# Performance work log

Measured on AMD Instinct MI355X. Metric: run time of the kernel, lower is better.

## Reference

```python
import jax, jax.numpy as jnp
import numpy as np
from jax import lax

EPS = 1e-12

def _ln(x, bias):
    # zero_mean=False, scale=False LayerNorm: RMS-style normalize + bias
    var = jnp.mean(x * x, axis=-1, keepdims=True)
    return x / jnp.sqrt(var + EPS) + bias

def _lru(h, nu_log, theta_log, b_re, b_im, c_re, c_im, d):
    # h: [B,S,H]; diagonal complex linear recurrence (LRU)
    lam = jnp.exp(-jnp.exp(nu_log) + 1j * jnp.exp(theta_log))  # [U] complex
    gamma = jnp.sqrt(jnp.clip(1.0 - jnp.abs(lam) ** 2, 0.0, None)).astype(h.dtype)  # [U]
    Bu = (jnp.einsum('bsh,uh->bsu', h, b_re) + 1j * jnp.einsum('bsh,uh->bsu', h, b_im)) * gamma  # [B,S,U]
    a = jnp.broadcast_to(lam, Bu.shape)
    def binop(e1, e2):
        a1, x1 = e1
        a2, x2 = e2
        return a1 * a2, a2 * x1 + x2
    _, states = lax.associative_scan(binop, (a, Bu), axis=1)  # [B,S,U] complex
    y = (jnp.einsum('bsu,hu->bsh', jnp.real(states), c_re)
         - jnp.einsum('bsu,hu->bsh', jnp.imag(states), c_im))
    return y + d * h

def setup_inputs() -> dict:
    key = jax.random.key(0)
    ks = jax.random.split(key, 12)
    B, S, H, L, F, V, P = 4, 2048, 1024, 4, 4096, 32000, 2048
    s = 0.02
    return {
        'input_ids': jax.random.randint(ks[0], (B, S), 0, V),
        'word_emb': jax.random.normal(ks[1], (V, H), jnp.float32) * s,
        'pos_emb': jax.random.normal(ks[2], (P, H), jnp.float32) * s,
        'nu_log': jax.random.normal(ks[3], (L, H), jnp.float32) * 0.5,
        'theta_log': jax.random.normal(ks[4], (L, H), jnp.float32) * 0.5,
        'B_re': jax.random.normal(ks[5], (L, H, H), jnp.float32) / np.sqrt(H),
        'B_im': jax.random.normal(ks[6], (L, H, H), jnp.float32) / np.sqrt(H),
        'C_re': jax.random.normal(ks[7], (L, H, H), jnp.float32) / np.sqrt(H),
        'C_im': jax.random.normal(ks[8], (L, H, H), jnp.float32) / np.sqrt(H),
        'D': jax.random.normal(ks[9], (L, H), jnp.float32),
        'rnn_norm_bias': jnp.zeros((L, H), jnp.float32),
        'w1': jax.random.normal(ks[10], (L, F, H), jnp.float32) * s,
        'b1': jnp.zeros((L, F), jnp.float32),
        'w2': jax.random.normal(ks[11], (L, H, F), jnp.float32) * s,
        'b2': jnp.zeros((L, H), jnp.float32),
        'ffn_norm_bias': jnp.zeros((L, H), jnp.float32),
    }

def reference(input_ids, word_emb, pos_emb, nu_log, theta_log, B_re, B_im,
              C_re, C_im, D, rnn_norm_bias, w1, b1, w2, b2, ffn_norm_bias):
    S = input_ids.shape[1]
    pos_ids = jnp.arange(S)
    h = word_emb[input_ids] + pos_emb[pos_ids][None, :, :]  # [B,S,H]
    L = nu_log.shape[0]
    for l in range(L):
        rnn_out = _lru(h, nu_log[l], theta_log[l], B_re[l], B_im[l], C_re[l], C_im[l], D[l])
        h = _ln(h + rnn_out, rnn_norm_bias[l])
        ffn = jnp.einsum('bsf,hf->bsh',
                         jax.nn.gelu(jnp.einsum('bsh,fh->bsf', h, w1[l]) + b1[l], approximate=False),
                         w2[l]) + b2[l]
        h = _ln(h + ffn, ffn_norm_bias[l])
    return h
```

## Files before the change

### kernel.cpp

```cpp
#include <hip/hip_runtime.h>
#include <hip/hip_bf16.h>
#include <math.h>

typedef __attribute__((ext_vector_type(8))) short short8;
typedef __attribute__((ext_vector_type(4))) float f32x4;

__device__ __forceinline__ float bf2f(unsigned short u) {
  union { unsigned int i; float f; } v; v.i = ((unsigned int)u) << 16; return v.f;
}
__device__ __forceinline__ unsigned short f2bf(float f) {
  union { float f; unsigned int i; } v; v.f = f;
  unsigned int r = v.i + 0x7fffu + ((v.i >> 16) & 1u);
  return (unsigned short)(r >> 16);
}
__device__ __forceinline__ uint4 cvt8(const float* __restrict__ src, float scale) {
  float4 a = *(const float4*)src;
  float4 b = *(const float4*)(src + 4);
  uint4 o; unsigned short* op = (unsigned short*)&o;
  op[0] = f2bf(a.x * scale); op[1] = f2bf(a.y * scale);
  op[2] = f2bf(a.z * scale); op[3] = f2bf(a.w * scale);
  op[4] = f2bf(b.x * scale); op[5] = f2bf(b.y * scale);
  op[6] = f2bf(b.z * scale); op[7] = f2bf(b.w * scale);
  return o;
}
__device__ __forceinline__ void glds16(const unsigned short* g, unsigned short* s) {
  __builtin_amdgcn_global_load_lds(
      (const __attribute__((address_space(1))) unsigned int*)g,
      (__attribute__((address_space(3))) unsigned int*)s, 16, 0, 0);
}

__global__ void embed_k(const int* __restrict__ ids, const float* __restrict__ we,
                        const float* __restrict__ pe, unsigned short* __restrict__ h) {
  int t = blockIdx.x * 256 + threadIdx.x;
  int c8 = (t & 127) * 8, row = t >> 7;
  int s = row & 2047;
  int id = ids[row];
  const float* ap = we + (size_t)id * 1024 + c8;
  const float* bp = pe + (size_t)s * 1024 + c8;
  float4 a0 = *(const float4*)ap, a1 = *(const float4*)(ap + 4);
  float4 b0 = *(const float4*)bp, b1 = *(const float4*)(bp + 4);
  uint4 o; unsigned short* op = (unsigned short*)&o;
  op[0] = f2bf(a0.x + b0.x); op[1] = f2bf(a0.y + b0.y);
  op[2] = f2bf(a0.z + b0.z); op[3] = f2bf(a0.w + b0.w);
  op[4] = f2bf(a1.x + b1.x); op[5] = f2bf(a1.y + b1.y);
  op[6] = f2bf(a1.z + b1.z); op[7] = f2bf(a1.w + b1.w);
  *(uint4*)(h + (size_t)row * 1024 + c8) = o;
}

__global__ void prep_lam_k(const float* __restrict__ nu_log,
                           const float* __restrict__ theta_log,
                           float* __restrict__ lamP) {
  int t = blockIdx.x * 256 + threadIdx.x;
  float nu = nu_log[t], th = theta_log[t];
  float mag = expf(-expf(nu));
  float eth = expf(th);
  float lr = mag * cosf(eth), li = mag * sinf(eth);
  float g2 = 1.0f - mag * mag; if (g2 < 0.f) g2 = 0.f;
  float pr = 1.f, pi = 0.f;
#pragma unroll 1
  for (int i = 0; i < 64; ++i) { float nr = pr * lr - pi * li; pi = pr * li + pi * lr; pr = nr; }
  lamP[t] = lr;
  lamP[4096 + t] = li;
  lamP[2 * 4096 + t] = sqrtf(g2);
  lamP[3 * 4096 + t] = pr;
  lamP[4 * 4096 + t] = pi;
}

__global__ void prep_w_k(const float* __restrict__ Bre, const float* __restrict__ Bim,
                         const float* __restrict__ Cre, const float* __restrict__ Cim,
                         const float* __restrict__ gamma, unsigned short* __restrict__ Bw,
                         unsigned short* __restrict__ Cw) {
  int t = blockIdx.x * 256 + threadIdx.x;
  if (t < 262144) {
    int n = t >> 7, h8 = (t & 127) * 8;
    int u = n & 1023;
    const float* src = (n < 1024 ? Bre : Bim) + (size_t)u * 1024 + h8;
    *(uint4*)(Bw + (size_t)n * 1024 + h8) = cvt8(src, gamma[u]);
  } else {
    int t2 = t - 262144;
    int hrow = t2 >> 8, u8 = (t2 & 255) * 8;
    uint4 o;
    if (u8 < 1024) o = cvt8(Cre + (size_t)hrow * 1024 + u8, 1.0f);
    else           o = cvt8(Cim + (size_t)hrow * 1024 + (u8 - 1024), -1.0f);
    *(uint4*)(Cw + (size_t)hrow * 2048 + u8) = o;
  }
}

__global__ void prep_ffn_k(const float* __restrict__ w1l, const float* __restrict__ w2l,
                           unsigned short* __restrict__ w1b, unsigned short* __restrict__ w2b) {
  int t = blockIdx.x * 256 + threadIdx.x;
  size_t off = (size_t)t * 8;
  if (t < 524288) {
    *(uint4*)(w1b + off) = cvt8(w1l + off, 1.0f);
  } else {
    size_t o2 = off - 4194304;
    *(uint4*)(w2b + o2) = cvt8(w2l + o2, 1.0f);
  }
}

template <int EPI>
__global__ __launch_bounds__(256, 2) void gemm_nt(
    const unsigned short* __restrict__ A, const unsigned short* __restrict__ Bm,
    void* __restrict__ Cout, const float* __restrict__ bias, int M, int N, int K) {
  __shared__ unsigned short As[2 * 128 * 32];
  __shared__ unsigned short Bs[2 * 128 * 32];
  const int tid = threadIdx.x;
  const int lane = tid & 63;
  const int wave = tid >> 6;
  const int quad = lane >> 4, r = lane & 15;
  const int wm = (wave >> 1) * 64, wn = (wave & 1) * 64;
  const size_t row0 = (size_t)blockIdx.x * 128;
  const size_t col0 = (size_t)blockIdx.y * 128;
  const unsigned short* Ab = A + row0 * K;
  const unsigned short* Bb = Bm + col0 * K;
  const int li0 = tid, li1 = 256 + tid;
  const int rw0 = li0 >> 2, sg0 = (li0 & 3) * 8;
  const int rw1 = li1 >> 2, sg1 = (li1 & 3) * 8;
  unsigned short* As0 = As + wave * 512;
  unsigned short* Bs0 = Bs + wave * 512;
  unsigned short* As1 = As + 2048 + wave * 512;
  unsigned short* Bs1 = Bs + 2048 + wave * 512;
  const unsigned short* Ap0 = Ab + (size_t)rw0 * K + sg0;
  const unsigned short* Bp0 = Bb + (size_t)rw0 * K + sg0;
  const unsigned short* Ap1 = Ab + (size_t)rw1 * K + sg1;
  const unsigned short* Bp1 = Bb + (size_t)rw1 * K + sg1;

  f32x4 acc[4][4];
#pragma unroll
  for (int i = 0; i < 4; ++i)
#pragma unroll
    for (int j = 0; j < 4; ++j) acc[i][j] = (f32x4){0.f, 0.f, 0.f, 0.f};

  glds16(Ap0, As0);
  glds16(Bp0, Bs0);
  glds16(Ap1, As1);
  glds16(Bp1, Bs1);
  __syncthreads();

  const int nk = K >> 5;
  int cur = 0;
  for (int t = 0; t < nk; ++t) {
    if (t + 1 < nk) {
      const int kn = (t + 1) << 5;
      const int nb = (cur ^ 1) * 4096;
      glds16(Ap0 + kn, As0 + nb);
      glds16(Bp0 + kn, Bs0 + nb);
      glds16(Ap1 + kn, As1 + nb);
      glds16(Bp1 + kn, Bs1 + nb);
    }
    const unsigned short* Ac = As + cur * 4096;
    const unsigned short* Bc = Bs + cur * 4096;
    short8 aF[4], bF[4];
#pragma unroll
    for (int i = 0; i < 4; ++i) aF[i] = *(const short8*)(Ac + (wm + i * 16 + r) * 32 + quad * 8);
#pragma unroll
    for (int j = 0; j < 4; ++j) bF[j] = *(const short8*)(Bc + (wn + j * 16 + r) * 32 + quad * 8);
#pragma unroll
    for (int i = 0; i < 4; ++i)
#pragma unroll
      for (int j = 0; j < 4; ++j)
        acc[i][j] = __builtin_amdgcn_mfma_f32_16x16x32_bf16(aF[i], bF[j], acc[i][j], 0, 0, 0);
    __syncthreads();
    cur ^= 1;
  }
  unsigned short* Cb = (unsigned short*)Cout;
  float* Cf = (float*)Cout;
#pragma unroll
  for (int j = 0; j < 4; ++j) {
    const size_t gcol = col0 + wn + j * 16 + r;
    float bv = 0.f;
    if (EPI == 2 || EPI == 3) bv = bias[gcol];
#pragma unroll
    for (int i = 0; i < 4; ++i) {
      const size_t grow = row0 + wm + i * 16 + quad * 4;
#pragma unroll
      for (int tt = 0; tt < 4; ++tt) {
        float v = acc[i][j][tt] + bv;
        size_t idx = (grow + tt) * (size_t)N + gcol;
        if (EPI == 2) {
          v = 0.5f * v * (1.0f + erff(v * 0.70710678118654752f));
          Cb[idx] = f2bf(v);
        } else if (EPI == 0) {
          Cb[idx] = f2bf(v);
        } else {
          Cf[idx] = v;
        }
      }
    }
  }
}

__global__ void scan_carry_k(const unsigned short* __restrict__ Bu, const float* __restrict__ lamP,
                             float* __restrict__ carry, int l) {
  int t = blockIdx.x * 256 + threadIdx.x;
  int u = t & 1023, c = (t >> 10) & 31, b = t >> 15;
  float lr = lamP[l * 1024 + u], li = lamP[4096 + l * 1024 + u];
  const unsigned short* base = Bu + ((size_t)(b * 2048 + c * 64)) * 2048 + u;
  float sr = 0.f, si = 0.f;
  for (int g = 0; g < 4; ++g) {
#pragma unroll
    for (int j = 0; j < 16; ++j) {
      size_t off = (size_t)(g * 16 + j) * 2048;
      float vr = bf2f(base[off]), vi = bf2f(base[off + 1024]);
      float nr = lr * sr - li * si + vr;
      si = lr * si + li * sr + vi;
      sr = nr;
    }
  }
  size_t idx = ((size_t)b * 32 + c) * 1024 + u;
  carry[idx] = sr; carry[131072 + idx] = si;
}

__global__ void scan_comb_k(const float* __restrict__ carry, const float* __restrict__ lamP,
                            float* __restrict__ inst, int l) {
  int t = blockIdx.x * 256 + threadIdx.x;
  int u = t & 1023, b = t >> 10;
  float tr = lamP[3 * 4096 + l * 1024 + u], ti = lamP[4 * 4096 + l * 1024 + u];
  float pr = 0.f, pi = 0.f;
  for (int c = 0; c < 32; ++c) {
    size_t idx = ((size_t)b * 32 + c) * 1024 + u;
    inst[idx] = pr; inst[131072 + idx] = pi;
    float cr = carry[idx], ci = carry[131072 + idx];
    float nr = tr * pr - ti * pi + cr;
    pi = tr * pi + ti * pr + ci;
    pr = nr;
  }
}

__global__ void scan_final_k(unsigned short* __restrict__ Bu, const float* __restrict__ lamP,
                             const float* __restrict__ inst, int l) {
  int t = blockIdx.x * 256 + threadIdx.x;
  int u = t & 1023, c = (t >> 10) & 31, b = t >> 15;
  float lr = lamP[l * 1024 + u], li = lamP[4096 + l * 1024 + u];
  size_t idx = ((size_t)b * 32 + c) * 1024 + u;
  float sr = inst[idx], si = inst[131072 + idx];
  unsigned short* base = Bu + ((size_t)(b * 2048 + c * 64)) * 2048 + u;
  for (int g = 0; g < 4; ++g) {
#pragma unroll
    for (int j = 0; j < 16; ++j) {
      size_t off = (size_t)(g * 16 + j) * 2048;
      float vr = bf2f(base[off]), vi = bf2f(base[off + 1024]);
      float nr = lr * sr - li * si + vr;
      si = lr * si + li * sr + vi;
      sr = nr;
      base[off] = f2bf(sr); base[off + 1024] = f2bf(si);
    }
  }
}

template <int HASD, int YF32, int OUTF32>
__global__ void ln_k(const unsigned short* __restrict__ h, const void* __restrict__ yv,
                     const float* __restrict__ Dv, const float* __restrict__ bias,
                     void* __restrict__ outv) {
  int wave = threadIdx.x >> 6, lane = threadIdx.x & 63;
  size_t row = (size_t)blockIdx.x * 4 + wave;
  const unsigned short* hr = h + row * 1024;
  float x[16]; float ss = 0.f;
#pragma unroll
  for (int cc = 0; cc < 2; ++cc) {
    int col = cc * 512 + lane * 8;
    uint4 hv = *(const uint4*)(hr + col);
    const unsigned short* hp = (const unsigned short*)&hv;
    float yf[8];
    if (YF32) {
      const float* yr = (const float*)yv + row * 1024 + col;
      float4 y0 = *(const float4*)yr, y1 = *(const float4*)(yr + 4);
      yf[0] = y0.x; yf[1] = y0.y; yf[2] = y0.z; yf[3] = y0.w;
      yf[4] = y1.x; yf[5] = y1.y; yf[6] = y1.z; yf[7] = y1.w;
    } else {
      uint4 yv4 = *(const uint4*)((const unsigned short*)yv + row * 1024 + col);
      const unsigned short* yp = (const unsigned short*)&yv4;
#pragma unroll
      for (int j = 0; j < 8; ++j) yf[j] = bf2f(yp[j]);
    }
    if (HASD) {
      const float* dp = Dv + col;
      float4 d0 = *(const float4*)dp, d1 = *(const float4*)(dp + 4);
      float df[8] = {d0.x, d0.y, d0.z, d0.w, d1.x, d1.y, d1.z, d1.w};
#pragma unroll
      for (int j = 0; j < 8; ++j) {
        float hf = bf2f(hp[j]);
        float v = hf + yf[j] + df[j] * hf;
        x[cc * 8 + j] = v; ss += v * v;
      }
    } else {
#pragma unroll
      for (int j = 0; j < 8; ++j) {
        float v = bf2f(hp[j]) + yf[j];
        x[cc * 8 + j] = v; ss += v * v;
      }
    }
  }
#pragma unroll
  for (int off = 32; off > 0; off >>= 1) ss += __shfl_xor(ss, off);
  float rs = rsqrtf(ss * (1.0f / 1024.0f) + 1e-12f);
#pragma unroll
  for (int cc = 0; cc < 2; ++cc) {
    int col = cc * 512 + lane * 8;
    const float* bp = bias + col;
    float4 b0 = *(const float4*)bp, b1 = *(const float4*)(bp + 4);
    float bf[8] = {b0.x, b0.y, b0.z, b0.w, b1.x, b1.y, b1.z, b1.w};
    if (OUTF32) {
      float* op = (float*)outv + row * 1024 + col;
      float4 o0, o1;
      o0.x = x[cc*8+0]*rs + bf[0]; o0.y = x[cc*8+1]*rs + bf[1];
      o0.z = x[cc*8+2]*rs + bf[2]; o0.w = x[cc*8+3]*rs + bf[3];
      o1.x = x[cc*8+4]*rs + bf[4]; o1.y = x[cc*8+5]*rs + bf[5];
      o1.z = x[cc*8+6]*rs + bf[6]; o1.w = x[cc*8+7]*rs + bf[7];
      *(float4*)op = o0; *(float4*)(op + 4) = o1;
    } else {
      uint4 o; unsigned short* op = (unsigned short*)&o;
#pragma unroll
      for (int j = 0; j < 8; ++j) op[j] = f2bf(x[cc * 8 + j] * rs + bf[j]);
      *(uint4*)((unsigned short*)outv + row * 1024 + col) = o;
    }
  }
}

extern "C" void kernel_launch(void* const* d_in, const int* in_sizes, int n_in,
                              void* d_out, int out_size, void* d_ws, size_t ws_size,
                              hipStream_t stream) {
  const int H = 1024, F = 4096;
  const int*   ids = (const int*)d_in[0];
  const float* we  = (const float*)d_in[1];
  const float* pe  = (const float*)d_in[2];
  const float* nu  = (const float*)d_in[3];
  const float* th  = (const float*)d_in[4];
  const float* Bre = (const float*)d_in[5];
  const float* Bim = (const float*)d_in[6];
  const float* Cre = (const float*)d_in[7];
  const float* Cim = (const float*)d_in[8];
  const float* Dv  = (const float*)d_in[9];
  const float* rnb = (const float*)d_in[10];
  const float* w1  = (const float*)d_in[11];
  const float* b1  = (const float*)d_in[12];
  const float* w2  = (const float*)d_in[13];
  const float* b2  = (const float*)d_in[14];
  const float* fnb = (const float*)d_in[15];
  float* out = (float*)d_out;

  char* w = (char*)d_ws;
  float* lamP  = (float*)w; w += (size_t)5 * 4096 * 4;
  float* carry = (float*)w; w += (size_t)2 * 131072 * 4;
  float* inst  = (float*)w; w += (size_t)2 * 131072 * 4;
  unsigned short* Bw   = (unsigned short*)w; w += (size_t)2048 * 1024 * 2;
  unsigned short* Cw   = (unsigned short*)w; w += (size_t)1024 * 2048 * 2;
  unsigned short* w1b  = (unsigned short*)w; w += (size_t)4096 * 1024 * 2;
  unsigned short* w2b  = (unsigned short*)w; w += (size_t)1024 * 4096 * 2;
  unsigned short* hcur = (unsigned short*)w; w += (size_t)8192 * 1024 * 2;
  unsigned short* Bu   = (unsigned short*)w;
  float*          facc = (float*)Bu;
  w += (size_t)8192 * 2048 * 2;
  unsigned short* ybt  = (unsigned short*)w; w += (size_t)8192 * 1024 * 2;
  unsigned short* t1   = (unsigned short*)w; w += (size_t)8192 * 4096 * 2;

  embed_k<<<4096, 256, 0, stream>>>(ids, we, pe, hcur);
  prep_lam_k<<<16, 256, 0, stream>>>(nu, th, lamP);

  for (int l = 0; l < 4; ++l) {
    prep_w_k<<<2048, 256, 0, stream>>>(Bre + (size_t)l * H * H, Bim + (size_t)l * H * H,
                                       Cre + (size_t)l * H * H, Cim + (size_t)l * H * H,
                                       lamP + 2 * 4096 + l * 1024, Bw, Cw);
    gemm_nt<0><<<dim3(64, 16), 256, 0, stream>>>(hcur, Bw, Bu, nullptr, 8192, 2048, 1024);
    scan_carry_k<<<512, 256, 0, stream>>>(Bu, lamP, carry, l);
    scan_comb_k<<<16, 256, 0, stream>>>(carry, lamP, inst, l);
    scan_final_k<<<512, 256, 0, stream>>>(Bu, lamP, inst, l);
    gemm_nt<0><<<dim3(64, 8), 256, 0, stream>>>(Bu, Cw, ybt, nullptr, 8192, 1024, 2048);
    ln_k<1, 0, 0><<<2048, 256, 0, stream>>>(hcur, ybt, Dv + l * H, rnb + l * H, hcur);
    prep_ffn_k<<<4096, 256, 0, stream>>>(w1 + (size_t)l * F * H, w2 + (size_t)l * H * F,
                                         w1b, w2b);
    gemm_nt<2><<<dim3(64, 32), 256, 0, stream>>>(hcur, w1b, t1,
                                                 b1 + (size_t)l * F, 8192, 4096, 1024);
    gemm_nt<3><<<dim3(64, 8), 256, 0, stream>>>(t1, w2b, facc, b2 + (size_t)l * H,
                                                8192, 1024, 4096);
    if (l == 3)
      ln_k<0, 1, 1><<<2048, 256, 0, stream>>>(hcur, facc, nullptr, fnb + l * H, out);
    else
      ln_k<0, 1, 0><<<2048, 256, 0, stream>>>(hcur, facc, nullptr, fnb + l * H, hcur);
  }
}
```

Before: 1.667 ms.

## Add 256x256-tile GEMM kernel and restructure LDS prefetch to two-stage-ahead

Adds a 512-thread GEMM kernel with 256x256 output tiles (8 waves, 128x64 per wave) and uses it for the LRU input projection and the FFN up-projection, so each loaded tile feeds more MFMAs. Both GEMM kernels now issue the global-to-LDS loads for tile t+2 after the barrier instead of tile t+1 before compute. They also raise wave priority around the MFMA block. The larger tiles raise register use and give fewer blocks (256 or 512) for 256 CUs. The prefetch reorder may expose load latency, since the next tile's load is only issued one iteration before it is consumed.

```diff
diff --git a/kernel.cpp b/kernel.cpp
--- a/kernel.cpp
+++ b/kernel.cpp
@@ -102,8 +102,8 @@
 __global__ __launch_bounds__(256, 2) void gemm_nt(
     const unsigned short* __restrict__ A, const unsigned short* __restrict__ Bm,
     void* __restrict__ Cout, const float* __restrict__ bias, int M, int N, int K) {
-  __shared__ unsigned short As[2 * 128 * 32];
-  __shared__ unsigned short Bs[2 * 128 * 32];
+  __shared__ __align__(16) unsigned short As[2 * 128 * 32];
+  __shared__ __align__(16) unsigned short Bs[2 * 128 * 32];
   const int tid = threadIdx.x;
   const int lane = tid & 63;
   const int wave = tid >> 6;
@@ -131,37 +131,37 @@
 #pragma unroll
     for (int j = 0; j < 4; ++j) acc[i][j] = (f32x4){0.f, 0.f, 0.f, 0.f};
 
-  glds16(Ap0, As0);
-  glds16(Bp0, Bs0);
-  glds16(Ap1, As1);
-  glds16(Bp1, Bs1);
+  glds16(Ap0, As0);       glds16(Bp0, Bs0);
+  glds16(Ap1, As1);       glds16(Bp1, Bs1);
+  glds16(Ap0 + 32, As0 + 4096); glds16(Bp0 + 32, Bs0 + 4096);
+  glds16(Ap1 + 32, As1 + 4096); glds16(Bp1 + 32, Bs1 + 4096);
   __syncthreads();
 
   const int nk = K >> 5;
-  int cur = 0;
   for (int t = 0; t < nk; ++t) {
-    if (t + 1 < nk) {
-      const int kn = (t + 1) << 5;
-      const int nb = (cur ^ 1) * 4096;
+    const unsigned short* Ac = As + (t & 1) * 4096;
+    const unsigned short* Bc = Bs + (t & 1) * 4096;
+    short8 aF[4], bF[4];
+#pragma unroll
+    for (int i = 0; i < 4; ++i) aF[i] = *(const short8*)(Ac + (wm + i * 16 + r) * 32 + quad * 8);
+#pragma unroll
+    for (int j = 0; j < 4; ++j) bF[j] = *(const short8*)(Bc + (wn + j * 16 + r) * 32 + quad * 8);
+    __builtin_amdgcn_s_setprio(1);
+#pragma unroll
+    for (int i = 0; i < 4; ++i)
+#pragma unroll
+      for (int j = 0; j < 4; ++j)
+        acc[i][j] = __builtin_amdgcn_mfma_f32_16x16x32_bf16(aF[i], bF[j], acc[i][j], 0, 0, 0);
+    __builtin_amdgcn_s_setprio(0);
+    __syncthreads();
+    if (t + 2 < nk) {
+      const int kn = (t + 2) << 5;
+      const int nb = (t & 1) * 4096;
       glds16(Ap0 + kn, As0 + nb);
       glds16(Bp0 + kn, Bs0 + nb);
       glds16(Ap1 + kn, As1 + nb);
       glds16(Bp1 + kn, Bs1 + nb);
     }
-    const unsigned short* Ac = As + cur * 4096;
-    const unsigned short* Bc = Bs + cur * 4096;
-    short8 aF[4], bF[4];
-#pragma unroll
-    for (int i = 0; i < 4; ++i) aF[i] = *(const short8*)(Ac + (wm + i * 16 + r) * 32 + quad * 8);
-#pragma unroll
-    for (int j = 0; j < 4; ++j) bF[j] = *(const short8*)(Bc + (wn + j * 16 + r) * 32 + quad * 8);
-#pragma unroll
-    for (int i = 0; i < 4; ++i)
-#pragma unroll
-      for (int j = 0; j < 4; ++j)
-        acc[i][j] = __builtin_amdgcn_mfma_f32_16x16x32_bf16(aF[i], bF[j], acc[i][j], 0, 0, 0);
-    __syncthreads();
-    cur ^= 1;
   }
   unsigned short* Cb = (unsigned short*)Cout;
   float* Cf = (float*)Cout;
@@ -177,6 +177,104 @@
       for (int tt = 0; tt < 4; ++tt) {
         float v = acc[i][j][tt] + bv;
         size_t idx = (grow + tt) * (size_t)N + gcol;
+        if (EPI == 2) {
+          v = 0.5f * v * (1.0f + erff(v * 0.70710678118654752f));
+          Cb[idx] = f2bf(v);
+        } else if (EPI == 0) {
+          Cb[idx] = f2bf(v);
+        } else {
+          Cf[idx] = v;
+        }
+      }
+    }
+  }
+}
+
+template <int EPI>
+__global__ __launch_bounds__(512, 2) void gemm256(
+    const unsigned short* __restrict__ A, const unsigned short* __restrict__ Bm,
+    void* __restrict__ Cout, const float* __restrict__ bias, int M, int N, int K) {
+  __shared__ __align__(16) unsigned short As[2 * 8192];
+  __shared__ __align__(16) unsigned short Bs[2 * 8192];
+  const int tid = threadIdx.x;
+  const int lane = tid & 63, wave = tid >> 6;
+  const int quad = lane >> 4, r = lane & 15;
+  const int wr = wave >> 2, wc = wave & 3;
+  const size_t row0 = (size_t)blockIdx.x * 256;
+  const size_t col0 = (size_t)blockIdx.y * 256;
+  const unsigned short* Ab = A + row0 * K;
+  const unsigned short* Bb = Bm + col0 * K;
+  const unsigned short* ApL = Ab + (size_t)(tid >> 2) * K + (tid & 3) * 8;
+  const unsigned short* BpL = Bb + (size_t)(tid >> 2) * K + (tid & 3) * 8;
+  const size_t rhalf = (size_t)128 * K;
+  const int arow = wr * 128 + r;
+  const int brow = wc * 64 + r;
+
+  f32x4 acc[8][4];
+#pragma unroll
+  for (int i = 0; i < 8; ++i)
+#pragma unroll
+    for (int j = 0; j < 4; ++j) acc[i][j] = (f32x4){0.f, 0.f, 0.f, 0.f};
+
+  const int nt = K >> 5;
+#pragma unroll
+  for (int d = 0; d < 2; ++d) {
+    const int k0 = d * 32;
+    unsigned short* ad = As + d * 8192 + wave * 512;
+    unsigned short* bd = Bs + d * 8192 + wave * 512;
+    glds16(ApL + k0, ad);
+    glds16(ApL + rhalf + k0, ad + 4096);
+    glds16(BpL + k0, bd);
+    glds16(BpL + rhalf + k0, bd + 4096);
+  }
+  __syncthreads();
+
+  for (int t = 0; t < nt; ++t) {
+    const unsigned short* Ac = As + (t & 1) * 8192;
+    const unsigned short* Bc = Bs + (t & 1) * 8192;
+    short8 aF[8], bF[4];
+#pragma unroll
+    for (int n = 0; n < 4; ++n)
+      bF[n] = *(const short8*)(Bc + (brow + n * 16) * 32 + quad * 8);
+#pragma unroll
+    for (int p = 0; p < 4; ++p) {
+      aF[2 * p]     = *(const short8*)(Ac + (arow + (2 * p) * 16) * 32 + quad * 8);
+      aF[2 * p + 1] = *(const short8*)(Ac + (arow + (2 * p + 1) * 16) * 32 + quad * 8);
+      __builtin_amdgcn_s_setprio(1);
+#pragma unroll
+      for (int mm = 0; mm < 2; ++mm)
+#pragma unroll
+        for (int n = 0; n < 4; ++n)
+          acc[2 * p + mm][n] = __builtin_amdgcn_mfma_f32_16x16x32_bf16(
+              aF[2 * p + mm], bF[n], acc[2 * p + mm][n], 0, 0, 0);
+      __builtin_amdgcn_s_setprio(0);
+    }
+    __syncthreads();
+    if (t + 2 < nt) {
+      const int k0 = (t + 2) * 32;
+      const int d = t & 1;
+      unsigned short* ad = As + d * 8192 + wave * 512;
+      unsigned short* bd = Bs + d * 8192 + wave * 512;
+      glds16(ApL + k0, ad);
+      glds16(ApL + rhalf + k0, ad + 4096);
+      glds16(BpL + k0, bd);
+      glds16(BpL + rhalf + k0, bd + 4096);
+    }
+  }
+  unsigned short* Cb = (unsigned short*)Cout;
+  float* Cf = (float*)Cout;
+#pragma unroll
+  for (int n = 0; n < 4; ++n) {
+    const size_t gcol = col0 + wc * 64 + n * 16 + r;
+    float bv = 0.f;
+    if (EPI == 2 || EPI == 3) bv = bias[gcol];
+#pragma unroll
+    for (int m = 0; m < 8; ++m) {
+      const size_t grow = row0 + wr * 128 + m * 16 + quad * 4;
+#pragma unroll
+      for (int tt2 = 0; tt2 < 4; ++tt2) {
+        float v = acc[m][n][tt2] + bv;
+        size_t idx = (grow + tt2) * (size_t)N + gcol;
         if (EPI == 2) {
           v = 0.5f * v * (1.0f + erff(v * 0.70710678118654752f));
           Cb[idx] = f2bf(v);
@@ -361,7 +459,7 @@
     prep_w_k<<<2048, 256, 0, stream>>>(Bre + (size_t)l * H * H, Bim + (size_t)l * H * H,
                                        Cre + (size_t)l * H * H, Cim + (size_t)l * H * H,
                                        lamP + 2 * 4096 + l * 1024, Bw, Cw);
-    gemm_nt<0><<<dim3(64, 16), 256, 0, stream>>>(hcur, Bw, Bu, nullptr, 8192, 2048, 1024);
+    gemm256<0><<<dim3(32, 8), 512, 0, stream>>>(hcur, Bw, Bu, nullptr, 8192, 2048, 1024);
     scan_carry_k<<<512, 256, 0, stream>>>(Bu, lamP, carry, l);
     scan_comb_k<<<16, 256, 0, stream>>>(carry, lamP, inst, l);
     scan_final_k<<<512, 256, 0, stream>>>(Bu, lamP, inst, l);
@@ -369,7 +467,7 @@
     ln_k<1, 0, 0><<<2048, 256, 0, stream>>>(hcur, ybt, Dv + l * H, rnb + l * H, hcur);
     prep_ffn_k<<<4096, 256, 0, stream>>>(w1 + (size_t)l * F * H, w2 + (size_t)l * H * F,
                                          w1b, w2b);
-    gemm_nt<2><<<dim3(64, 32), 256, 0, stream>>>(hcur, w1b, t1,
+    gemm256<2><<<dim3(32, 16), 512, 0, stream>>>(hcur, w1b, t1,
                                                  b1 + (size_t)l * F, 8192, 4096, 1024);
     gemm_nt<3><<<dim3(64, 8), 256, 0, stream>>>(t1, w2b, facc, b2 + (size_t)l * H,
                                                 8192, 1024, 4096);
```

After: 1.739 ms. 1.04x slower.

## Triple-buffer GEMM LDS tiles with vmcnt waits and single barrier per step

Applied to the files above, without the earlier changes.

The bf16 GEMM kernel moves from a double-buffered to a triple-buffered LDS pipeline, prefetching two K-tiles ahead with direct global-to-LDS loads. Each step waits with explicit s_waitcnt vmcnt and uses one barrier instead of a trailing __syncthreads. It also raises wave priority around the MFMA block with s_setprio. The aim is to hide global load latency and cut synchronisation stalls, at the cost of 50% more LDS per block, which could reduce occupancy or add risk in the hand-written wait counts.

```diff
diff --git a/kernel.cpp b/kernel.cpp
--- a/kernel.cpp
+++ b/kernel.cpp
@@ -102,8 +102,8 @@
 __global__ __launch_bounds__(256, 2) void gemm_nt(
     const unsigned short* __restrict__ A, const unsigned short* __restrict__ Bm,
     void* __restrict__ Cout, const float* __restrict__ bias, int M, int N, int K) {
-  __shared__ unsigned short As[2 * 128 * 32];
-  __shared__ unsigned short Bs[2 * 128 * 32];
+  __shared__ __align__(16) unsigned short As[3 * 4096];
+  __shared__ __align__(16) unsigned short Bs[3 * 4096];
   const int tid = threadIdx.x;
   const int lane = tid & 63;
   const int wave = tid >> 6;
@@ -116,14 +116,11 @@
   const int li0 = tid, li1 = 256 + tid;
   const int rw0 = li0 >> 2, sg0 = (li0 & 3) * 8;
   const int rw1 = li1 >> 2, sg1 = (li1 & 3) * 8;
-  unsigned short* As0 = As + wave * 512;
-  unsigned short* Bs0 = Bs + wave * 512;
-  unsigned short* As1 = As + 2048 + wave * 512;
-  unsigned short* Bs1 = Bs + 2048 + wave * 512;
   const unsigned short* Ap0 = Ab + (size_t)rw0 * K + sg0;
   const unsigned short* Bp0 = Bb + (size_t)rw0 * K + sg0;
   const unsigned short* Ap1 = Ab + (size_t)rw1 * K + sg1;
   const unsigned short* Bp1 = Bb + (size_t)rw1 * K + sg1;
+  const int woff = wave * 512;
 
   f32x4 acc[4][4];
 #pragma unroll
@@ -131,22 +128,30 @@
 #pragma unroll
     for (int j = 0; j < 4; ++j) acc[i][j] = (f32x4){0.f, 0.f, 0.f, 0.f};
 
-  glds16(Ap0, As0);
-  glds16(Bp0, Bs0);
-  glds16(Ap1, As1);
-  glds16(Bp1, Bs1);
-  __syncthreads();
-
   const int nk = K >> 5;
+  {
+    glds16(Ap0, As + woff);            glds16(Bp0, Bs + woff);
+    glds16(Ap1, As + woff + 2048);     glds16(Bp1, Bs + woff + 2048);
+    glds16(Ap0 + 32, As + 4096 + woff);        glds16(Bp0 + 32, Bs + 4096 + woff);
+    glds16(Ap1 + 32, As + 4096 + woff + 2048); glds16(Bp1 + 32, Bs + 4096 + woff + 2048);
+  }
+
   int cur = 0;
   for (int t = 0; t < nk; ++t) {
     if (t + 1 < nk) {
-      const int kn = (t + 1) << 5;
-      const int nb = (cur ^ 1) * 4096;
-      glds16(Ap0 + kn, As0 + nb);
-      glds16(Bp0 + kn, Bs0 + nb);
-      glds16(Ap1 + kn, As1 + nb);
-      glds16(Bp1 + kn, Bs1 + nb);
+      asm volatile("s_waitcnt vmcnt(4)" ::: "memory");
+    } else {
+      asm volatile("s_waitcnt vmcnt(0)" ::: "memory");
+    }
+    __builtin_amdgcn_s_barrier();
+    asm volatile("" ::: "memory");
+    if (t + 2 < nk) {
+      int stb = cur - 1; if (stb < 0) stb += 3;
+      const int k0 = (t + 2) << 5;
+      unsigned short* ad = As + stb * 4096 + woff;
+      unsigned short* bd = Bs + stb * 4096 + woff;
+      glds16(Ap0 + k0, ad);          glds16(Bp0 + k0, bd);
+      glds16(Ap1 + k0, ad + 2048);   glds16(Bp1 + k0, bd + 2048);
     }
     const unsigned short* Ac = As + cur * 4096;
     const unsigned short* Bc = Bs + cur * 4096;
@@ -155,13 +160,14 @@
     for (int i = 0; i < 4; ++i) aF[i] = *(const short8*)(Ac + (wm + i * 16 + r) * 32 + quad * 8);
 #pragma unroll
     for (int j = 0; j < 4; ++j) bF[j] = *(const short8*)(Bc + (wn + j * 16 + r) * 32 + quad * 8);
+    __builtin_amdgcn_s_setprio(1);
 #pragma unroll
     for (int i = 0; i < 4; ++i)
 #pragma unroll
       for (int j = 0; j < 4; ++j)
         acc[i][j] = __builtin_amdgcn_mfma_f32_16x16x32_bf16(aF[i], bF[j], acc[i][j], 0, 0, 0);
-    __syncthreads();
-    cur ^= 1;
+    __builtin_amdgcn_s_setprio(0);
+    cur = (cur == 2) ? 0 : cur + 1;
   }
   unsigned short* Cb = (unsigned short*)Cout;
   float* Cf = (float*)Cout;
```

Result: slower. 1.723 ms (+3.4%).
